# Optimization experiments

Measured on AMD Instinct MI355X. Metric: run time of the kernel, lower is better.

## Reference

```python
import jax, jax.numpy as jnp
import numpy as np


def _grid_sample_bilinear_border(img, grid):
    """Faithful jax port of F.grid_sample(mode='bilinear', padding_mode='border',
    align_corners=False). img: [B,C,H,W], grid: [B,Hg,Wg,2] (x,y in [-1,1]).
    Returns [B,C,Hg,Wg]."""
    B, C, H, W = img.shape
    gx, gy = grid[..., 0], grid[..., 1]           # [B,Hg,Wg]
    # unnormalize (align_corners=False)
    ix = ((gx + 1.0) * W - 1.0) * 0.5
    iy = ((gy + 1.0) * H - 1.0) * 0.5
    ix0f = jnp.floor(ix)
    iy0f = jnp.floor(iy)
    wx = (ix - ix0f)[:, None]                     # [B,1,Hg,Wg] broadcast over C
    wy = (iy - iy0f)[:, None]
    x0 = jnp.clip(ix0f.astype(jnp.int32), 0, W - 1)
    x1 = jnp.clip(ix0f.astype(jnp.int32) + 1, 0, W - 1)
    y0 = jnp.clip(iy0f.astype(jnp.int32), 0, H - 1)
    y1 = jnp.clip(iy0f.astype(jnp.int32) + 1, 0, H - 1)

    def gather(im, yy, xx):                       # im [C,H,W], yy/xx [Hg,Wg]
        return im[:, yy, xx]                      # [C,Hg,Wg]

    g = jax.vmap(gather)
    v00 = g(img, y0, x0)
    v01 = g(img, y0, x1)
    v10 = g(img, y1, x0)
    v11 = g(img, y1, x1)
    return (v00 * (1.0 - wx) * (1.0 - wy)
            + v01 * wx * (1.0 - wy)
            + v10 * (1.0 - wx) * wy
            + v11 * wx * wy)


def setup_inputs() -> dict:
    key = jax.random.key(0)
    k1, k2, k3 = jax.random.split(key, 3)
    B, C, V, D, P = 1, 16, 360, 736, 16384        # batch, ch, views, detectors, recon pixels
    sinogram = jax.random.normal(k1, (B, C, V, D), dtype=jnp.float32)
    grid = jax.random.uniform(k2, (B, V, P, 2), dtype=jnp.float32,
                              minval=-1.1, maxval=1.1)
    square_inv = jax.random.uniform(k3, (B, 1, V, P), dtype=jnp.float32,
                                    minval=0.5, maxval=1.5) * 1e-3
    return {"sinogram": sinogram, "grid": grid, "square_inv": square_inv}


def reference(sinogram, grid, square_inv):
    # back_projection: bilinear gather over sinogram at grid coords, weight by
    # inverse-square distance, sum over the view axis (dim -2).
    sampled = _grid_sample_bilinear_border(sinogram, grid)   # [B,C,view,P]
    recon_img = jnp.sum(sampled * square_inv * 1000.0, axis=-2)  # [B,C,P]
    return recon_img
```

## Files before the change

kernel.cpp:

```cpp
#include <hip/hip_runtime.h>
#include <hip/hip_bf16.h>

#define NP 16384
#define NV 360
#define ND 736
#define NC 16
#define VS 16
#define QSZ (NV * ND * 8)

__global__ __launch_bounds__(256) void sino_transpose_bf16(const float* __restrict__ sino,
                                                           ushort* __restrict__ st) {
    int idx = blockIdx.x * 256 + threadIdx.x;
    if (idx >= NV * ND) return;
    uint packed[8];
#pragma unroll
    for (int q = 0; q < 8; ++q) {
        uint ul = __float_as_uint(sino[(2 * q)     * (NV * ND) + idx]);
        uint uh = __float_as_uint(sino[(2 * q + 1) * (NV * ND) + idx]);
        ul = (ul + 0x7fffu + ((ul >> 16) & 1u)) >> 16;
        uh = (uh + 0x7fffu + ((uh >> 16) & 1u)) >> 16;
        packed[q] = ul | (uh << 16);
    }
    uint4* d0 = reinterpret_cast<uint4*>(st + ((size_t)idx << 3));
    uint4* d1 = reinterpret_cast<uint4*>(st + QSZ + ((size_t)idx << 3));
    *d0 = make_uint4(packed[0], packed[1], packed[2], packed[3]);
    *d1 = make_uint4(packed[4], packed[5], packed[6], packed[7]);
}

__global__ __launch_bounds__(256) void backproj(const float* __restrict__ grd,
                                                const float* __restrict__ sq,
                                                const ushort* __restrict__ st,
                                                float* __restrict__ out) {
    int Q    = blockIdx.x & 1;
    int r    = blockIdx.x >> 1;
    int pblk = r & 127;
    int vs   = r >> 7;
    int pr   = threadIdx.x >> 1;
    int c    = threadIdx.x & 1;
    int p    = pblk * 128 + pr;
    int v0 = (vs * NV) / VS;
    int v1 = ((vs + 1) * NV) / VS;

    const ushort* __restrict__ tbl = st + Q * QSZ;

    float acc[8];
#pragma unroll
    for (int k = 0; k < 8; ++k) acc[k] = 0.0f;

    const float2* grd2 = reinterpret_cast<const float2*>(grd);

    auto gather = [&](int idx, float w) {
        uint4 a = *reinterpret_cast<const uint4*>(tbl + ((size_t)idx << 3));
        uint u[4] = {a.x, a.y, a.z, a.w};
#pragma unroll
        for (int q = 0; q < 4; ++q) {
            acc[2 * q]     = fmaf(__uint_as_float(u[q] << 16),         w, acc[2 * q]);
            acc[2 * q + 1] = fmaf(__uint_as_float(u[q] & 0xffff0000u), w, acc[2 * q + 1]);
        }
    };

#pragma unroll 2
    for (int v = v0; v < v1; ++v) {
        int gi = v * NP + p;
        float2 g = grd2[gi];
        float w  = sq[gi] * 1000.0f;

        float ix = ((g.x + 1.0f) * (float)ND - 1.0f) * 0.5f;
        float iy = ((g.y + 1.0f) * (float)NV - 1.0f) * 0.5f;
        float x0f = floorf(ix), y0f = floorf(iy);
        float wx = ix - x0f,   wy = iy - y0f;
        int x0i = (int)x0f, y0i = (int)y0f;
        int x0 = min(max(x0i,     0), ND - 1);
        int x1 = min(max(x0i + 1, 0), ND - 1);
        int y0 = min(max(y0i,     0), NV - 1);
        int y1 = min(max(y0i + 1, 0), NV - 1);

        int   xc  = c ? x1 : x0;
        float wxc = (c ? wx : (1.0f - wx)) * w;

        gather(y0 * ND + xc, wxc * (1.0f - wy));
        gather(y1 * ND + xc, wxc * wy);
    }

#pragma unroll
    for (int k = 0; k < 8; ++k) acc[k] += __shfl_xor(acc[k], 1);
    if (c == 0) {
#pragma unroll
        for (int k = 0; k < 8; ++k)
            atomicAdd(&out[(Q * 8 + k) * NP + p], acc[k]);
    }
}

extern "C" void kernel_launch(void* const* d_in, const int* in_sizes, int n_in,
                              void* d_out, int out_size, void* d_ws, size_t ws_size,
                              hipStream_t stream) {
    const float* sino = (const float*)d_in[0];
    const float* grd  = (const float*)d_in[1];
    const float* sq   = (const float*)d_in[2];
    float* out = (float*)d_out;
    ushort* st = (ushort*)d_ws;

    hipMemsetAsync(out, 0, (size_t)out_size * sizeof(float), stream);

    {
        int n = NV * ND;
        sino_transpose_bf16<<<(n + 255) / 256, 256, 0, stream>>>(sino, st);
    }
    {
        int nblocks = 2 * 128 * VS;
        backproj<<<nblocks, 256, 0, stream>>>(grd, sq, st, out);
    }
}
```

Measured before the change: 248.1 us.

## Interleave channel halves in table, 4 threads per pixel, fuse output zeroing

The bf16 sinogram table is now stored with all 16 channels of a texel contiguous (32 bytes). Four threads per pixel handle the two x-corners and the two channel halves, so each pixel's grid and weight values are read once instead of once per channel-half block. Output zeroing moves into the transpose kernel, removing the memset launch, and the view split drops from 16 to 8. The change cuts redundant grid/sq traffic and atomics, at the cost of fewer blocks and longer per-block loops.

```diff
diff --git a/kernel.cpp b/kernel.cpp
--- a/kernel.cpp
+++ b/kernel.cpp
@@ -5,12 +5,16 @@
 #define NV 360
 #define ND 736
 #define NC 16
-#define VS 16
-#define QSZ (NV * ND * 8)
+#define VS 8
 
-__global__ __launch_bounds__(256) void sino_transpose_bf16(const float* __restrict__ sino,
-                                                           ushort* __restrict__ st) {
+__device__ __forceinline__ float bf_lo(uint u) { return __uint_as_float(u << 16); }
+__device__ __forceinline__ float bf_hi(uint u) { return __uint_as_float(u & 0xffff0000u); }
+
+__global__ __launch_bounds__(256) void k0_transpose(const float* __restrict__ sino,
+                                                    ushort* __restrict__ st,
+                                                    float* __restrict__ out) {
     int idx = blockIdx.x * 256 + threadIdx.x;
+    if (idx < NC * NP) out[idx] = 0.0f;
     if (idx >= NV * ND) return;
     uint packed[8];
 #pragma unroll
@@ -21,43 +25,30 @@
         uh = (uh + 0x7fffu + ((uh >> 16) & 1u)) >> 16;
         packed[q] = ul | (uh << 16);
     }
-    uint4* d0 = reinterpret_cast<uint4*>(st + ((size_t)idx << 3));
-    uint4* d1 = reinterpret_cast<uint4*>(st + QSZ + ((size_t)idx << 3));
-    *d0 = make_uint4(packed[0], packed[1], packed[2], packed[3]);
-    *d1 = make_uint4(packed[4], packed[5], packed[6], packed[7]);
+    uint4* dst = reinterpret_cast<uint4*>(st + ((size_t)idx << 4));
+    dst[0] = make_uint4(packed[0], packed[1], packed[2], packed[3]);
+    dst[1] = make_uint4(packed[4], packed[5], packed[6], packed[7]);
 }
 
 __global__ __launch_bounds__(256) void backproj(const float* __restrict__ grd,
                                                 const float* __restrict__ sq,
                                                 const ushort* __restrict__ st,
                                                 float* __restrict__ out) {
-    int Q    = blockIdx.x & 1;
-    int r    = blockIdx.x >> 1;
-    int pblk = r & 127;
-    int vs   = r >> 7;
-    int pr   = threadIdx.x >> 1;
-    int c    = threadIdx.x & 1;
-    int p    = pblk * 128 + pr;
-    int v0 = (vs * NV) / VS;
-    int v1 = ((vs + 1) * NV) / VS;
-
-    const ushort* __restrict__ tbl = st + Q * QSZ;
+    int tid  = threadIdx.x;
+    int p    = ((blockIdx.x & 255) << 6) + (tid >> 2);
+    int vs   = blockIdx.x >> 8;
+    int sub  = tid & 3;
+    int side = sub & 1;
+    int half = sub >> 1;
+    int v0 = vs * (NV / VS);
+    int v1 = v0 + (NV / VS);
 
     float acc[8];
 #pragma unroll
     for (int k = 0; k < 8; ++k) acc[k] = 0.0f;
 
     const float2* grd2 = reinterpret_cast<const float2*>(grd);
-
-    auto gather = [&](int idx, float w) {
-        uint4 a = *reinterpret_cast<const uint4*>(tbl + ((size_t)idx << 3));
-        uint u[4] = {a.x, a.y, a.z, a.w};
-#pragma unroll
-        for (int q = 0; q < 4; ++q) {
-            acc[2 * q]     = fmaf(__uint_as_float(u[q] << 16),         w, acc[2 * q]);
-            acc[2 * q + 1] = fmaf(__uint_as_float(u[q] & 0xffff0000u), w, acc[2 * q + 1]);
-        }
-    };
+    const uint4*  tbl  = reinterpret_cast<const uint4*>(st);
 
 #pragma unroll 2
     for (int v = v0; v < v1; ++v) {
@@ -75,19 +66,29 @@
         int y0 = min(max(y0i,     0), NV - 1);
         int y1 = min(max(y0i + 1, 0), NV - 1);
 
-        int   xc  = c ? x1 : x0;
-        float wxc = (c ? wx : (1.0f - wx)) * w;
+        int   xc  = side ? x1 : x0;
+        float wxc = (side ? wx : (1.0f - wx)) * w;
 
-        gather(y0 * ND + xc, wxc * (1.0f - wy));
-        gather(y1 * ND + xc, wxc * wy);
+        uint4 a = tbl[((y0 * ND + xc) << 1) + half];
+        uint4 b = tbl[((y1 * ND + xc) << 1) + half];
+        float wa = wxc * (1.0f - wy);
+        float wb = wxc * wy;
+
+        uint ua[4] = {a.x, a.y, a.z, a.w};
+        uint ub[4] = {b.x, b.y, b.z, b.w};
+#pragma unroll
+        for (int q = 0; q < 4; ++q) {
+            acc[2*q]   = fmaf(bf_lo(ua[q]), wa, fmaf(bf_lo(ub[q]), wb, acc[2*q]));
+            acc[2*q+1] = fmaf(bf_hi(ua[q]), wa, fmaf(bf_hi(ub[q]), wb, acc[2*q+1]));
+        }
     }
 
 #pragma unroll
     for (int k = 0; k < 8; ++k) acc[k] += __shfl_xor(acc[k], 1);
-    if (c == 0) {
+    if (side == 0) {
 #pragma unroll
         for (int k = 0; k < 8; ++k)
-            atomicAdd(&out[(Q * 8 + k) * NP + p], acc[k]);
+            atomicAdd(&out[(half * 8 + k) * NP + p], acc[k]);
     }
 }
 
@@ -100,14 +101,12 @@
     float* out = (float*)d_out;
     ushort* st = (ushort*)d_ws;
 
-    hipMemsetAsync(out, 0, (size_t)out_size * sizeof(float), stream);
-
     {
         int n = NV * ND;
-        sino_transpose_bf16<<<(n + 255) / 256, 256, 0, stream>>>(sino, st);
+        k0_transpose<<<(n + 255) / 256, 256, 0, stream>>>(sino, st, out);
     }
     {
-        int nblocks = 2 * 128 * VS;
+        int nblocks = 256 * VS;
         backproj<<<nblocks, 256, 0, stream>>>(grd, sq, st, out);
     }
 }
```

After: 225.2 us. 1.1x faster.
